# Kernel tuning notes

Measured on AMD Instinct MI355X. Metric: run time of the kernel, lower is better.

The kernel has to match this reference:

```python
import jax, jax.numpy as jnp
import numpy as np
from math import factorial, sqrt

E_EDGES = 65536
N_NODES = 4096
F_HID = 64
MUL = 64
EPSILON = 0.25
P_ENV = 6.0

# ---- real Clebsch-Gordan (e3nn-style w3j, unit Frobenius norm) ----

def _su2_cg(j1, j2, j3, m1, m2, m3):
    if m3 != m1 + m2:
        return 0.0
    f = factorial
    pref = sqrt((2 * j3 + 1) * f(j3 + j1 - j2) * f(j3 - j1 + j2) * f(j1 + j2 - j3) / f(j1 + j2 + j3 + 1))
    pref *= sqrt(f(j3 + m3) * f(j3 - m3) * f(j1 - m1) * f(j1 + m1) * f(j2 - m2) * f(j2 + m2))
    s = 0.0
    for k in range(0, j1 + j2 - j3 + 1):
        d = [k, j1 + j2 - j3 - k, j1 - m1 - k, j2 + m2 - k, j3 - j2 + m1 + k, j3 - j1 - m2 + k]
        if min(d) < 0:
            continue
        den = 1.0
        for t in d:
            den *= f(t)
        s += (-1.0) ** k / den
    return pref * s

def _qmat(l):  # real -> complex change of basis, [complex m, real m]
    q = np.zeros((2 * l + 1, 2 * l + 1), dtype=np.complex128)
    for m in range(-l, 0):
        q[l + m, l + abs(m)] = 1.0 / sqrt(2)
        q[l + m, l - abs(m)] = -1j / sqrt(2)
    q[l, l] = 1.0
    for m in range(1, l + 1):
        q[l + m, l + abs(m)] = (-1) ** m / sqrt(2)
        q[l + m, l - abs(m)] = 1j * (-1) ** m / sqrt(2)
    return (-1j) ** l * q

def _w3j(l1, l2, l3):
    C = np.zeros((2 * l1 + 1, 2 * l2 + 1, 2 * l3 + 1), dtype=np.complex128)
    for i, m1 in enumerate(range(-l1, l1 + 1)):
        for j, m2 in enumerate(range(-l2, l2 + 1)):
            for k, m3 in enumerate(range(-l3, l3 + 1)):
                C[i, j, k] = _su2_cg(l1, l2, l3, m1, m2, m3)
    Cr = np.einsum('ai,bj,ck,abc->ijk', _qmat(l1), _qmat(l2), np.conj(_qmat(l3)), C)
    Cr = np.real(Cr)
    return (Cr / np.linalg.norm(Cr)).astype(np.float32)

_PATH_KEYS = [(0,0,0),(1,1,0),(2,2,0),(0,1,1),(1,0,1),(1,2,1),(2,1,1),(3,2,1),(0,2,2),(1,1,2),(2,0,2),(2,2,2),(3,1,2),(2,1,3)]
_W3J_NP = {k: _w3j(*k) for k in _PATH_KEYS}

def _sh_consts():  # normalization so ||Y_l||^2 = 2l+1 (component norm)
    u = np.array([0.3, -0.4, sqrt(0.75)])
    y1 = sqrt(3.0) * u
    y2r = np.einsum('i,j,ijk->k', y1, y1, _W3J_NP[(1, 1, 2)])
    c2 = sqrt(5.0) / np.linalg.norm(y2r)
    y3r = np.einsum('i,j,ijk->k', c2 * y2r, y1, _W3J_NP[(2, 1, 3)])
    c3 = sqrt(7.0) / np.linalg.norm(y3r)
    return float(c2), float(c3)

_C2, _C3 = _sh_consts()
_W3J = {k: jnp.asarray(v) for k, v in _W3J_NP.items()}


def _sph(u):  # component-normalized real SH l=0..3 via CG recursion, u unit [E,3]
    y0 = jnp.ones_like(u[:, :1])
    y1 = jnp.sqrt(jnp.float32(3.0)) * u
    y2 = _C2 * jnp.einsum('ei,ej,ijk->ek', y1, y1, _W3J[(1, 1, 2)])
    y3 = _C3 * jnp.einsum('ei,ej,ijk->ek', y2, y1, _W3J[(2, 1, 3)])
    return jnp.concatenate([y0, y1, y2, y3], axis=1)  # [E, 16]


def _tp(a, b, key):  # per-mul CG product path, component normalization
    l3 = key[2]
    return jnp.sqrt(jnp.float32(2 * l3 + 1)) * jnp.einsum('eui,euj,ijk->euk', a, b, _W3J[key])


def _forward(vectors, x, V, Ww, W1, W2, W3, Wl1, Wl2, senders):
    E = vectors.shape[0]
    lengths = jnp.linalg.norm(vectors, axis=1)  # [E]
    u = vectors / (lengths[:, None] + 1e-12)
    Y = _sph(u)  # [E, 16]
    # two-body MLP (single linear, no act), e3nn 1/sqrt(fan_in) scaling
    w = (x @ Ww) / jnp.sqrt(jnp.float32(x.shape[1]))  # [E, MUL]
    # weighted SH, scatter_sum over senders, map back to edges
    M = w[:, :, None] * Y[:, None, :]  # [E, MUL, 16]
    wY = jax.ops.segment_sum(M, senders, num_segments=N_NODES)[senders] * EPSILON
    wY0, wY1, wY2, wY3 = wY[..., 0:1], wY[..., 1:4], wY[..., 4:9], wY[..., 9:16]
    V0 = V[:, :MUL].reshape(E, MUL, 1)
    V1 = V[:, MUL:4 * MUL].reshape(E, MUL, 3)
    V2 = V[:, 4 * MUL:9 * MUL].reshape(E, MUL, 5)
    # CG tensor product wY(0e+1o+2e+3o) x V(0e+1o+2e), filtered to 0e+1o+2e
    S = jnp.concatenate([_tp(wY0, V0, (0, 0, 0)), _tp(wY1, V1, (1, 1, 0)), _tp(wY2, V2, (2, 2, 0))], axis=1)[..., 0]  # [E, 3*MUL]
    P = jnp.concatenate([_tp(wY0, V1, (0, 1, 1)), _tp(wY1, V0, (1, 0, 1)), _tp(wY1, V2, (1, 2, 1)), _tp(wY2, V1, (2, 1, 1)), _tp(wY3, V2, (3, 2, 1))], axis=1)  # [E, 5*MUL, 3]
    D = jnp.concatenate([_tp(wY0, V2, (0, 2, 2)), _tp(wY1, V1, (1, 1, 2)), _tp(wY2, V0, (2, 0, 2)), _tp(wY2, V2, (2, 2, 2)), _tp(wY3, V1, (3, 1, 2))], axis=1)  # [E, 5*MUL, 5]
    # scalars join the invariant track; latent MLP (silu x2, last linear)
    h = jnp.concatenate([x, S], axis=1)  # [E, F_HID + 3*MUL]
    h = jax.nn.silu(h @ W1 / jnp.sqrt(jnp.float32(h.shape[1])))
    h = jax.nn.silu(h @ W2 / jnp.sqrt(jnp.float32(F_HID)))
    h = h @ W3 / jnp.sqrt(jnp.float32(F_HID))
    # polynomial smoothing envelope (cutoff = 1)
    p = P_ENV
    d = lengths
    env = 1.0 - (p + 1.0) * (p + 2.0) / 2.0 * d ** 6 + p * (p + 2.0) * d ** 7 - p * (p + 1.0) / 2.0 * d ** 8
    env = jnp.where(d < 1.0, env, 0.0)
    x_out = env[:, None] * h  # [E, F_HID]
    # equivariant Linear to 64x1o + 64x2e (0e dropped: no path)
    nin = jnp.sqrt(jnp.float32(P.shape[1]))
    V1o = jnp.einsum('evi,vu->eui', P, Wl1) / nin  # [E, MUL, 3]
    V2e = jnp.einsum('evi,vu->eui', D, Wl2) / nin  # [E, MUL, 5]
    return jnp.concatenate([x_out, V1o.reshape(E, 3 * MUL), V2e.reshape(E, 5 * MUL)], axis=1)  # [E, 576]


def setup_inputs() -> dict:
    key = jax.random.key(0)
    ks = jax.random.split(key, 11)
    v = jax.random.normal(ks[0], (E_EDGES, 3), dtype=jnp.float32)
    r = 0.2 + 0.75 * jax.random.uniform(ks[1], (E_EDGES, 1), dtype=jnp.float32)
    vectors = v / (jnp.linalg.norm(v, axis=1, keepdims=True) + 1e-9) * r  # lengths in (0.2, 0.95)
    x = jax.random.normal(ks[2], (E_EDGES, F_HID), dtype=jnp.float32)
    V = jax.random.normal(ks[3], (E_EDGES, 9 * MUL), dtype=jnp.float32)
    senders = jax.random.randint(ks[4], (E_EDGES,), 0, N_NODES)
    Ww = jax.random.normal(ks[5], (F_HID, MUL), dtype=jnp.float32)
    W1 = jax.random.normal(ks[6], (F_HID + 3 * MUL, F_HID), dtype=jnp.float32)
    W2 = jax.random.normal(ks[7], (F_HID, F_HID), dtype=jnp.float32)
    W3 = jax.random.normal(ks[8], (F_HID, F_HID), dtype=jnp.float32)
    Wl1 = jax.random.normal(ks[9], (5 * MUL, MUL), dtype=jnp.float32)
    Wl2 = jax.random.normal(ks[10], (5 * MUL, MUL), dtype=jnp.float32)
    return {"vectors": vectors, "x": x, "V": V, "senders": senders, "Ww": Ww, "W1": W1, "W2": W2, "W3": W3, "Wl1": Wl1, "Wl2": Wl2}


def reference(vectors, x, V, senders, Ww, W1, W2, W3, Wl1, Wl2):
    return _forward(vectors, x, V, Ww, W1, W2, W3, Wl1, Wl2, senders)
```

## Files before the change

kernel.cpp:

```cpp
#include <hip/hip_runtime.h>

#define E_EDGES 65536
#define N_NODES 4096

#define WS_W     1024
#define WS_Y     (WS_W + E_EDGES*64)
#define WS_CNT   (WS_Y + E_EDGES*16)
#define WS_OFF   (WS_CNT + N_NODES)
#define WS_CUR   (WS_OFF + N_NODES)
#define WS_SORT  (WS_CUR + N_NODES)
#define WS_A     (WS_SORT + E_EDGES)

typedef __bf16 bf16x8 __attribute__((ext_vector_type(8)));
typedef float  f32x4  __attribute__((ext_vector_type(4)));

#define PK_WL   0
#define PK_W1   10240
#define PK_W2   14336
#define PK_W3   15360

__constant__ int gK_L1[14] = {0,1,2,0,1,1,2,3,0,1,2,2,3,2};
__constant__ int gK_L2[14] = {0,1,2,1,0,2,1,2,2,1,0,2,1,1};
__constant__ int gK_L3[14] = {0,0,0,1,1,1,1,1,2,2,2,2,2,3};
__constant__ int gK_OFF[14]= {0,1,10,35,44,53,98,143,248,273,318,343,468,573};
__constant__ double gFact[8] = {1.,1.,2.,6.,24.,120.,720.,5040.};

#define O_W000 0
#define O_W110 1
#define O_W220 10
#define O_W011 35
#define O_W101 44
#define O_W121 53
#define O_W211 98
#define O_W321 143
#define O_W022 248
#define O_W112 273
#define O_W202 318
#define O_W222 343
#define O_W312 468
#define O_W213 573

__device__ double su2_cg(int j1,int j2,int j3,int m1,int m2,int m3){
  if (m3 != m1+m2) return 0.0;
  double pref = sqrt((double)(2*j3+1)*gFact[j3+j1-j2]*gFact[j3-j1+j2]*gFact[j1+j2-j3]/gFact[j1+j2+j3+1]);
  pref *= sqrt(gFact[j3+m3]*gFact[j3-m3]*gFact[j1-m1]*gFact[j1+m1]*gFact[j2-m2]*gFact[j2+m2]);
  double s=0.0;
  for(int k=0;k<=j1+j2-j3;k++){
    int d1=j1+j2-j3-k, d2=j1-m1-k, d3=j2+m2-k, d4=j3-j2+m1+k, d5=j3-j1-m2+k;
    if(d1<0||d2<0||d3<0||d4<0||d5<0) continue;
    double den=gFact[k]*gFact[d1]*gFact[d2]*gFact[d3]*gFact[d4]*gFact[d5];
    s += (k&1)? (-1.0/den) : (1.0/den);
  }
  return pref*s;
}

__device__ void fill_qmat(int l, double2* q){
  for(int i=0;i<49;i++){ q[i].x=0.0; q[i].y=0.0; }
  const double is2 = 0.7071067811865475244;
  for(int m=-l;m<0;m++){
    q[(l+m)*7+(l-m)].x = is2;
    q[(l+m)*7+(l+m)].y = -is2;
  }
  q[l*7+l].x = 1.0;
  for(int m=1;m<=l;m++){
    double sg = (m&1)? -1.0 : 1.0;
    q[(l+m)*7+(l+m)].x = sg*is2;
    q[(l+m)*7+(l-m)].y = sg*is2;
  }
  double pr, pi;
  switch(l&3){ case 0: pr=1;pi=0;break; case 1: pr=0;pi=-1;break; case 2: pr=-1;pi=0;break; default: pr=0;pi=1;break; }
  for(int i=0;i<49;i++){
    double a=q[i].x, b=q[i].y;
    q[i].x = a*pr - b*pi;
    q[i].y = a*pi + b*pr;
  }
}

__global__ __launch_bounds__(128) void k_w3j(float* __restrict__ ws){
  __shared__ double2 q1[49], q2[49], q3[49];
  __shared__ double C[125], Cr[125];
  __shared__ double red[128];
  int bid = blockIdx.x, t = threadIdx.x;
  int l1=gK_L1[bid], l2=gK_L2[bid], l3=gK_L3[bid];
  int n1=2*l1+1, n2=2*l2+1, n3=2*l3+1, ntot=n1*n2*n3;
  if(t==0){
    fill_qmat(l1,q1); fill_qmat(l2,q2); fill_qmat(l3,q3);
    for(int i=0;i<49;i++) q3[i].y = -q3[i].y;
  }
  __syncthreads();
  for(int idx=t; idx<ntot; idx+=128){
    int a = idx/(n2*n3), r=idx%(n2*n3), b=r/n3, c=r%n3;
    C[idx] = su2_cg(l1,l2,l3, a-l1, b-l2, c-l3);
  }
  __syncthreads();
  for(int idx=t; idx<ntot; idx+=128){
    int i = idx/(n2*n3), r=idx%(n2*n3), j=r/n3, k=r%n3;
    double ar=0.0;
    for(int a=0;a<n1;a++) for(int b=0;b<n2;b++){
      double2 qa=q1[a*7+i], qb=q2[b*7+j];
      double pr = qa.x*qb.x - qa.y*qb.y;
      double pi = qa.x*qb.y + qa.y*qb.x;
      for(int c=0;c<n3;c++){
        double2 qc=q3[c*7+k];
        double tr = pr*qc.x - pi*qc.y;
        ar += tr*C[(a*n2+b)*n3+c];
      }
    }
    Cr[idx]=ar;
  }
  __syncthreads();
  double ss=0.0;
  for(int idx=t; idx<ntot; idx+=128) ss += Cr[idx]*Cr[idx];
  red[t]=ss; __syncthreads();
  for(int st=64; st>0; st>>=1){ if(t<st) red[t]+=red[t+st]; __syncthreads(); }
  double inv = 1.0/sqrt(red[0]);
  for(int idx=t; idx<ntot; idx+=128) ws[gK_OFF[bid]+idx] = (float)(Cr[idx]*inv);
}

__global__ void k_c2c3(float* __restrict__ ws){
  const float* w112 = ws + O_W112;
  const float* w213 = ws + O_W213;
  double u0=0.3, u1=-0.4, u2=sqrt(0.75);
  double s3=sqrt(3.0);
  double y1[3]={s3*u0, s3*u1, s3*u2};
  double y2r[5]={0,0,0,0,0};
  for(int i=0;i<3;i++) for(int j=0;j<3;j++) for(int k=0;k<5;k++)
    y2r[k] += y1[i]*y1[j]*(double)w112[(i*3+j)*5+k];
  double nn=0; for(int k=0;k<5;k++) nn += y2r[k]*y2r[k];
  double c2 = sqrt(5.0)/sqrt(nn);
  double y2[5]; for(int k=0;k<5;k++) y2[k]=c2*y2r[k];
  double y3r[7]={0,0,0,0,0,0,0};
  for(int i=0;i<5;i++) for(int j=0;j<3;j++) for(int n=0;n<7;n++)
    y3r[n] += y2[i]*y1[j]*(double)w213[(i*3+j)*7+n];
  nn=0; for(int n=0;n<7;n++) nn += y3r[n]*y3r[n];
  double c3 = sqrt(7.0)/sqrt(nn);
  ws[678]=(float)c2; ws[679]=(float)c3;
}

__global__ void k_zero(int* __restrict__ cnt){
  int i = blockIdx.x*256 + threadIdx.x;
  if(i < N_NODES) cnt[i]=0;
}
__global__ void k_count(const int* __restrict__ senders, int* __restrict__ cnt){
  int e = blockIdx.x*256 + threadIdx.x;
  if(e < E_EDGES) atomicAdd(&cnt[senders[e]], 1);
}
__global__ __launch_bounds__(1024) void k_scan(const int* __restrict__ cnt, int* __restrict__ off, int* __restrict__ cur){
  __shared__ int part[1024];
  int t = threadIdx.x;
  int c0=cnt[4*t], c1=cnt[4*t+1], c2=cnt[4*t+2], c3=cnt[4*t+3];
  int l0=0, l1=c0, l2=c0+c1, l3=c0+c1+c2;
  int sum=l3+c3;
  part[t]=sum; __syncthreads();
  for(int st=1; st<1024; st<<=1){
    int v = part[t];
    int add = (t>=st)? part[t-st] : 0;
    __syncthreads();
    part[t] = v + add;
    __syncthreads();
  }
  int pref = (t>0)? part[t-1] : 0;
  off[4*t]=pref+l0; off[4*t+1]=pref+l1; off[4*t+2]=pref+l2; off[4*t+3]=pref+l3;
  cur[4*t]=pref+l0; cur[4*t+1]=pref+l1; cur[4*t+2]=pref+l2; cur[4*t+3]=pref+l3;
}
__global__ void k_scatter(const int* __restrict__ senders, int* __restrict__ cur, int* __restrict__ sorted){
  int e = blockIdx.x*256 + threadIdx.x;
  if(e < E_EDGES){
    int pos = atomicAdd(&cur[senders[e]], 1);
    sorted[pos] = e;
  }
}

__global__ __launch_bounds__(256) void k_wpack(
    const float* __restrict__ Wl1, const float* __restrict__ Wl2,
    const float* __restrict__ W1, const float* __restrict__ W2,
    const float* __restrict__ W3, float* __restrict__ wpk){
  int idx = blockIdx.x*256 + threadIdx.x;
  int lane = idx & 63;
  const float* W; int part, ks, nt;
  if(idx < PK_W1){
    nt = (idx>>6)&3; int rest = idx>>8; ks = rest%10; int mp = rest/10;
    part = mp&1; W = (mp>>1)? Wl2 : Wl1;
  } else if(idx < PK_W2){
    int rel = idx - PK_W1; part = rel>>11; int r2 = rel & 2047;
    ks = r2>>8; nt = (r2>>6)&3; W = W1;
  } else if(idx < PK_W3){
    int rel = idx - PK_W2; part = rel>>9; int r2 = rel & 511;
    ks = r2>>8; nt = (r2>>6)&3; W = W2;
  } else {
    int rel = idx - PK_W3; part = rel>>9; int r2 = rel & 511;
    ks = r2>>8; nt = (r2>>6)&3; W = W3;
  }
  int c = nt*16 + (lane & 15);
  int g = lane >> 4;
  bf16x8 outv;
  #pragma unroll
  for(int j=0;j<8;j++){
    int k = ks*32 + g*8 + j;
    float v = W[k*64 + c];
    __bf16 hb = (__bf16)v;
    outv[j] = part ? (__bf16)(v - (float)hb) : hb;
  }
  ((bf16x8*)wpk)[idx] = outv;
}

__global__ __launch_bounds__(256) void k_edge_pre(
    const float* __restrict__ vectors, const float* __restrict__ x,
    const float* __restrict__ Ww, float* __restrict__ ws){
  int wv = threadIdx.x >> 6, lane = threadIdx.x & 63;
  int e = blockIdx.x*4 + wv;
  const float* w112 = ws + O_W112;
  const float* w213 = ws + O_W213;
  float C2v = ws[678], C3v = ws[679];
  float v0=vectors[e*3], v1=vectors[e*3+1], v2=vectors[e*3+2];
  float len = sqrtf(v0*v0+v1*v1+v2*v2);
  float inv = 1.0f/(len + 1e-12f);
  float s3 = 1.7320508075688772f;
  float y1v[3] = { s3*v0*inv, s3*v1*inv, s3*v2*inv };
  float y2[5];
  #pragma unroll
  for(int k=0;k<5;k++){
    float a=0.f;
    #pragma unroll
    for(int i=0;i<3;i++)
      #pragma unroll
      for(int j=0;j<3;j++) a += y1v[i]*y1v[j]*w112[(i*3+j)*5+k];
    y2[k]=C2v*a;
  }
  float y3[7];
  #pragma unroll
  for(int n=0;n<7;n++){
    float a=0.f;
    #pragma unroll
    for(int i=0;i<5;i++)
      #pragma unroll
      for(int j=0;j<3;j++) a += y2[i]*y1v[j]*w213[(i*3+j)*7+n];
    y3[n]=C3v*a;
  }
  float acc=0.f;
  const float4* xp4 = (const float4*)(x + e*64);
  #pragma unroll
  for(int k4=0;k4<16;k4++){
    float4 xv = xp4[k4];
    acc += xv.x*Ww[(k4*4+0)*64+lane];
    acc += xv.y*Ww[(k4*4+1)*64+lane];
    acc += xv.z*Ww[(k4*4+2)*64+lane];
    acc += xv.w*Ww[(k4*4+3)*64+lane];
  }
  ws[WS_W + e*64 + lane] = acc*0.125f;
  if(lane==0){
    float* Yp = ws + WS_Y + e*16;
    Yp[0]=1.0f;
    Yp[1]=y1v[0]; Yp[2]=y1v[1]; Yp[3]=y1v[2];
    Yp[4]=y2[0]; Yp[5]=y2[1]; Yp[6]=y2[2]; Yp[7]=y2[3]; Yp[8]=y2[4];
    Yp[9]=y3[0]; Yp[10]=y3[1]; Yp[11]=y3[2]; Yp[12]=y3[3]; Yp[13]=y3[4]; Yp[15]=y3[6]; Yp[14]=y3[5];
  }
}

__global__ __launch_bounds__(64) void k_node_acc(
    const float* __restrict__ ws_w, const float* __restrict__ ws_y,
    const int* __restrict__ sorted, const int* __restrict__ off, const int* __restrict__ cnt,
    float* __restrict__ A){
  int n = blockIdx.x, m = threadIdx.x;
  float acc[16];
  #pragma unroll
  for(int k=0;k<16;k++) acc[k]=0.f;
  int o = off[n], c = cnt[n];
  for(int j=0;j<c;j++){
    int e = sorted[o+j];
    float wm = ws_w[e*64+m];
    const float4* Yp4 = (const float4*)(ws_y + e*16);
    float4 y0=Yp4[0], y1=Yp4[1], y2=Yp4[2], y3=Yp4[3];
    acc[0] += wm*y0.x; acc[1] += wm*y0.y; acc[2] += wm*y0.z; acc[3] += wm*y0.w;
    acc[4] += wm*y1.x; acc[5] += wm*y1.y; acc[6] += wm*y1.z; acc[7] += wm*y1.w;
    acc[8] += wm*y2.x; acc[9] += wm*y2.y; acc[10]+= wm*y2.z; acc[11]+= wm*y2.w;
    acc[12]+= wm*y3.x; acc[13]+= wm*y3.y; acc[14]+= wm*y3.z; acc[15]+= wm*y3.w;
  }
  float4* outp = (float4*)(A + n*1024 + m*16);
  outp[0] = make_float4(acc[0]*0.25f, acc[1]*0.25f, acc[2]*0.25f, acc[3]*0.25f);
  outp[1] = make_float4(acc[4]*0.25f, acc[5]*0.25f, acc[6]*0.25f, acc[7]*0.25f);
  outp[2] = make_float4(acc[8]*0.25f, acc[9]*0.25f, acc[10]*0.25f, acc[11]*0.25f);
  outp[3] = make_float4(acc[12]*0.25f, acc[13]*0.25f, acc[14]*0.25f, acc[15]*0.25f);
}

__device__ inline void split1(float v, __bf16& h, __bf16& l){
  h = (__bf16)v;
  l = (__bf16)(v - (float)h);
}

__global__ __launch_bounds__(256, 3) void k_main(
    const float* __restrict__ vectors, const float* __restrict__ x, const float* __restrict__ V,
    const int* __restrict__ senders,
    const float* __restrict__ ws, const int* __restrict__ sorted,
    float* __restrict__ out){
  __shared__ __align__(16) __bf16 lds_pdh[32*328];
  __shared__ __align__(16) __bf16 lds_pdl[32*328];
  __shared__ __align__(16) __bf16 lds_hh[4*264];
  __shared__ __align__(16) __bf16 lds_hl[4*264];
  __shared__ __align__(16) __bf16 lds_h1h[4*72];
  __shared__ __align__(16) __bf16 lds_h1l[4*72];
  __shared__ __align__(16) __bf16 lds_h2h[4*72];
  __shared__ __align__(16) __bf16 lds_h2l[4*72];
  __shared__ float lds_env[4];
  __shared__ int   lds_eid[4];

  int t = threadIdx.x;
  int wv = t>>6, lane = t&63;
  int eid = sorted[blockIdx.x*4 + wv];
  if(lane==0) lds_eid[wv]=eid;
  __syncthreads();

  const float* lw = ws;
  {
    float v0=vectors[eid*3], v1=vectors[eid*3+1], v2=vectors[eid*3+2];
    float d = sqrtf(v0*v0+v1*v1+v2*v2);
    float d2=d*d, d4=d2*d2, d6=d4*d2, d7=d6*d, d8=d7*d;
    float env = 1.0f - 28.0f*d6 + 48.0f*d7 - 21.0f*d8;
    env = (d < 1.0f) ? env : 0.0f;
    if(lane==0) lds_env[wv]=env;
  }
  int snd = senders[eid];
  const float4* Ap4 = (const float4*)(ws + WS_A + snd*1024 + lane*16);
  float4 a0=Ap4[0], a1=Ap4[1], a2=Ap4[2], a3=Ap4[3];
  float wY[16] = {a0.x,a0.y,a0.z,a0.w, a1.x,a1.y,a1.z,a1.w,
                  a2.x,a2.y,a2.z,a2.w, a3.x,a3.y,a3.z,a3.w};
  const float* Vp = V + eid*576;
  float V0 = Vp[lane];
  float V1f[3], V2f[5];
  #pragma unroll
  for(int i=0;i<3;i++) V1f[i]=Vp[64+lane*3+i];
  #pragma unroll
  for(int j=0;j<5;j++) V2f[j]=Vp[256+lane*5+j];
  {
    __bf16 hh, hl;
    split1(x[eid*64+lane], hh, hl);
    lds_hh[wv*264 + lane] = hh; lds_hl[wv*264 + lane] = hl;
  }
  float s0 = wY[0]*V0*lw[O_W000];
  float s1 = 0.f;
  #pragma unroll
  for(int i=0;i<3;i++)
    #pragma unroll
    for(int j=0;j<3;j++) s1 += wY[1+i]*V1f[j]*lw[O_W110 + i*3+j];
  float s2 = 0.f;
  #pragma unroll
  for(int i=0;i<5;i++)
    #pragma unroll
    for(int j=0;j<5;j++) s2 += wY[4+i]*V2f[j]*lw[O_W220 + i*5+j];
  {
    __bf16 hh, hl;
    split1(s0, hh, hl); lds_hh[wv*264+ 64+lane]=hh; lds_hl[wv*264+ 64+lane]=hl;
    split1(s1, hh, hl); lds_hh[wv*264+128+lane]=hh; lds_hl[wv*264+128+lane]=hl;
    split1(s2, hh, hl); lds_hh[wv*264+192+lane]=hh; lds_hl[wv*264+192+lane]=hl;
  }
  float P0[3]={0,0,0}, P1[3]={0,0,0}, P2[3]={0,0,0}, P3[3]={0,0,0}, P4[3]={0,0,0};
  float D0[5]={0,0,0,0,0}, D1[5]={0,0,0,0,0}, D2[5]={0,0,0,0,0}, D3[5]={0,0,0,0,0}, D4[5]={0,0,0,0,0};
  #pragma unroll
  for(int b=0;b<3;b++){ float pb=wY[0]*V1f[b];
    #pragma unroll
    for(int i=0;i<3;i++) P0[i]+= pb*lw[O_W011 + b*3+i]; }
  #pragma unroll
  for(int a=0;a<3;a++){ float pa=wY[1+a]*V0;
    #pragma unroll
    for(int i=0;i<3;i++) P1[i]+= pa*lw[O_W101 + a*3+i]; }
  #pragma unroll
  for(int a=0;a<3;a++)
    #pragma unroll
    for(int b=0;b<5;b++){ float p=wY[1+a]*V2f[b];
      #pragma unroll
      for(int i=0;i<3;i++) P2[i]+= p*lw[O_W121 + (a*5+b)*3+i]; }
  #pragma unroll
  for(int a=0;a<5;a++)
    #pragma unroll
    for(int b=0;b<3;b++){ float p=wY[4+a]*V1f[b];
      #pragma unroll
      for(int i=0;i<3;i++) P3[i]+= p*lw[O_W211 + (a*3+b)*3+i]; }
  #pragma unroll
  for(int a=0;a<7;a++)
    #pragma unroll
    for(int b=0;b<5;b++){ float p=wY[9+a]*V2f[b];
      #pragma unroll
      for(int i=0;i<3;i++) P4[i]+= p*lw[O_W321 + (a*5+b)*3+i]; }
  #pragma unroll
  for(int b=0;b<5;b++){ float pb=wY[0]*V2f[b];
    #pragma unroll
    for(int j=0;j<5;j++) D0[j]+= pb*lw[O_W022 + b*5+j]; }
  #pragma unroll
  for(int a=0;a<3;a++)
    #pragma unroll
    for(int b=0;b<3;b++){ float p=wY[1+a]*V1f[b];
      #pragma unroll
      for(int j=0;j<5;j++) D1[j]+= p*lw[O_W112 + (a*3+b)*5+j]; }
  #pragma unroll
  for(int a=0;a<5;a++){ float pa=wY[4+a]*V0;
    #pragma unroll
    for(int j=0;j<5;j++) D2[j]+= pa*lw[O_W202 + a*5+j]; }
  #pragma unroll
  for(int a=0;a<5;a++)
    #pragma unroll
    for(int b=0;b<5;b++){ float p=wY[4+a]*V2f[b];
      #pragma unroll
      for(int j=0;j<5;j++) D3[j]+= p*lw[O_W222 + (a*5+b)*5+j]; }
  #pragma unroll
  for(int a=0;a<7;a++)
    #pragma unroll
    for(int b=0;b<3;b++){ float p=wY[9+a]*V1f[b];
      #pragma unroll
      for(int j=0;j<5;j++) D4[j]+= p*lw[O_W312 + (a*3+b)*5+j]; }
  {
    const float SQ3 = 1.7320508075688772f, SQ5 = 2.2360679774997896f;
    #pragma unroll
    for(int i=0;i<3;i++){
      int row = wv*3+i;
      float vals[5] = {SQ3*P0[i], SQ3*P1[i], SQ3*P2[i], SQ3*P3[i], SQ3*P4[i]};
      #pragma unroll
      for(int p=0;p<5;p++){
        __bf16 h,l; split1(vals[p],h,l);
        lds_pdh[row*328 + p*64 + lane] = h;
        lds_pdl[row*328 + p*64 + lane] = l;
      }
    }
    #pragma unroll
    for(int j=0;j<5;j++){
      int row = 12 + wv*5 + j;
      float vals[5] = {SQ5*D0[j], SQ5*D1[j], SQ5*D2[j], SQ5*D3[j], SQ5*D4[j]};
      #pragma unroll
      for(int p=0;p<5;p++){
        __bf16 h,l; split1(vals[p],h,l);
        lds_pdh[row*328 + p*64 + lane] = h;
        lds_pdl[row*328 + p*64 + lane] = l;
      }
    }
  }
  __syncthreads();

  int g = lane >> 4, r = lane & 15;
  const bf16x8* WB = (const bf16x8*)(ws + WS_W);

  {
    int he = r & 3;
    f32x4 acc = {0.f,0.f,0.f,0.f};
    #pragma unroll
    for(int ks=0; ks<8; ks++){
      bf16x8 ah = *(const bf16x8*)(lds_hh + he*264 + ks*32 + g*8);
      bf16x8 al = *(const bf16x8*)(lds_hl + he*264 + ks*32 + g*8);
      bf16x8 bh = WB[PK_W1        + (ks*4+wv)*64 + lane];
      bf16x8 bl = WB[PK_W1 + 2048 + (ks*4+wv)*64 + lane];
      acc = __builtin_amdgcn_mfma_f32_16x16x32_bf16(ah, bh, acc, 0,0,0);
      acc = __builtin_amdgcn_mfma_f32_16x16x32_bf16(ah, bl, acc, 0,0,0);
      acc = __builtin_amdgcn_mfma_f32_16x16x32_bf16(al, bh, acc, 0,0,0);
    }
    if(g==0){
      #pragma unroll
      for(int e_=0;e_<4;e_++){
        float a = acc[e_]*(1.0f/16.0f);
        float h1 = a/(1.0f+__expf(-a));
        __bf16 hh,hl; split1(h1,hh,hl);
        lds_h1h[e_*72 + wv*16 + r] = hh;
        lds_h1l[e_*72 + wv*16 + r] = hl;
      }
    }
    __syncthreads();
    acc = (f32x4){0.f,0.f,0.f,0.f};
    #pragma unroll
    for(int ks=0; ks<2; ks++){
      bf16x8 ah = *(const bf16x8*)(lds_h1h + he*72 + ks*32 + g*8);
      bf16x8 al = *(const bf16x8*)(lds_h1l + he*72 + ks*32 + g*8);
      bf16x8 bh = WB[PK_W2       + (ks*4+wv)*64 + lane];
      bf16x8 bl = WB[PK_W2 + 512 + (ks*4+wv)*64 + lane];
      acc = __builtin_amdgcn_mfma_f32_16x16x32_bf16(ah, bh, acc, 0,0,0);
      acc = __builtin_amdgcn_mfma_f32_16x16x32_bf16(ah, bl, acc, 0,0,0);
      acc = __builtin_amdgcn_mfma_f32_16x16x32_bf16(al, bh, acc, 0,0,0);
    }
    if(g==0){
      #pragma unroll
      for(int e_=0;e_<4;e_++){
        float a = acc[e_]*0.125f;
        float h2 = a/(1.0f+__expf(-a));
        __bf16 hh,hl; split1(h2,hh,hl);
        lds_h2h[e_*72 + wv*16 + r] = hh;
        lds_h2l[e_*72 + wv*16 + r] = hl;
      }
    }
    __syncthreads();
    acc = (f32x4){0.f,0.f,0.f,0.f};
    #pragma unroll
    for(int ks=0; ks<2; ks++){
      bf16x8 ah = *(const bf16x8*)(lds_h2h + he*72 + ks*32 + g*8);
      bf16x8 al = *(const bf16x8*)(lds_h2l + he*72 + ks*32 + g*8);
      bf16x8 bh = WB[PK_W3       + (ks*4+wv)*64 + lane];
      bf16x8 bl = WB[PK_W3 + 512 + (ks*4+wv)*64 + lane];
      acc = __builtin_amdgcn_mfma_f32_16x16x32_bf16(ah, bh, acc, 0,0,0);
      acc = __builtin_amdgcn_mfma_f32_16x16x32_bf16(ah, bl, acc, 0,0,0);
      acc = __builtin_amdgcn_mfma_f32_16x16x32_bf16(al, bh, acc, 0,0,0);
    }
    if(g==0){
      #pragma unroll
      for(int e_=0;e_<4;e_++)
        out[lds_eid[e_]*576 + wv*16 + r] = lds_env[e_]*acc[e_]*0.125f;
    }
  }

  {
    f32x4 accP  = {0.f,0.f,0.f,0.f};
    f32x4 accD0 = {0.f,0.f,0.f,0.f};
    f32x4 accD1 = {0.f,0.f,0.f,0.f};
    int rP  = (r < 12) ? r : 11;
    int rD0 = 12 + r;
    int rD1 = 12 + ((r < 4) ? (16 + r) : 19);
    const __bf16* pPh  = lds_pdh + rP *328 + g*8;
    const __bf16* pPl  = lds_pdl + rP *328 + g*8;
    const __bf16* pD0h = lds_pdh + rD0*328 + g*8;
    const __bf16* pD0l = lds_pdl + rD0*328 + g*8;
    const __bf16* pD1h = lds_pdh + rD1*328 + g*8;
    const __bf16* pD1l = lds_pdl + rD1*328 + g*8;
    #pragma unroll 2
    for(int ks=0; ks<10; ks++){
      int bbase = (ks*4 + wv)*64 + lane;
      bf16x8 b1h = WB[bbase];
      bf16x8 b1l = WB[bbase + 2560];
      bf16x8 b2h = WB[bbase + 5120];
      bf16x8 b2l = WB[bbase + 7680];
      bf16x8 aPh  = *(const bf16x8*)(pPh  + ks*32);
      bf16x8 aPl  = *(const bf16x8*)(pPl  + ks*32);
      bf16x8 aD0h = *(const bf16x8*)(pD0h + ks*32);
      bf16x8 aD0l = *(const bf16x8*)(pD0l + ks*32);
      bf16x8 aD1h = *(const bf16x8*)(pD1h + ks*32);
      bf16x8 aD1l = *(const bf16x8*)(pD1l + ks*32);
      accP  = __builtin_amdgcn_mfma_f32_16x16x32_bf16(aPh,  b1h, accP,  0,0,0);
      accP  = __builtin_amdgcn_mfma_f32_16x16x32_bf16(aPh,  b1l, accP,  0,0,0);
      accP  = __builtin_amdgcn_mfma_f32_16x16x32_bf16(aPl,  b1h, accP,  0,0,0);
      accD0 = __builtin_amdgcn_mfma_f32_16x16x32_bf16(aD0h, b2h, accD0, 0,0,0);
      accD0 = __builtin_amdgcn_mfma_f32_16x16x32_bf16(aD0h, b2l, accD0, 0,0,0);
      accD0 = __builtin_amdgcn_mfma_f32_16x16x32_bf16(aD0l, b2h, accD0, 0,0,0);
      accD1 = __builtin_amdgcn_mfma_f32_16x16x32_bf16(aD1h, b2h, accD1, 0,0,0);
      accD1 = __builtin_amdgcn_mfma_f32_16x16x32_bf16(aD1h, b2l, accD1, 0,0,0);
      accD1 = __builtin_amdgcn_mfma_f32_16x16x32_bf16(aD1l, b2h, accD1, 0,0,0);
    }
    const float sc = 0.05590169943749474f;
    int u = wv*16 + r;
    if(g < 3){
      #pragma unroll
      for(int reg=0; reg<4; reg++){
        int R = g*4 + reg;
        int e_ = R/3, i_ = R - e_*3;
        out[lds_eid[e_]*576 + 64 + u*3 + i_] = accP[reg]*sc;
      }
    }
    #pragma unroll
    for(int reg=0; reg<4; reg++){
      int Dr = g*4 + reg;
      int e_ = Dr/5, j_ = Dr - e_*5;
      out[lds_eid[e_]*576 + 256 + u*5 + j_] = accD0[reg]*sc;
    }
    if(g == 0){
      #pragma unroll
      for(int reg=0; reg<4; reg++){
        int Dr = 16 + reg;
        int e_ = Dr/5, j_ = Dr - e_*5;
        out[lds_eid[e_]*576 + 256 + u*5 + j_] = accD1[reg]*sc;
      }
    }
  }
}

extern "C" void kernel_launch(void* const* d_in, const int* in_sizes, int n_in,
                              void* d_out, int out_size, void* d_ws, size_t ws_size,
                              hipStream_t stream) {
  const float* vectors=(const float*)d_in[0];
  const float* x      =(const float*)d_in[1];
  const float* V      =(const float*)d_in[2];
  const int*   senders=(const int*)  d_in[3];
  const float* Ww     =(const float*)d_in[4];
  const float* W1     =(const float*)d_in[5];
  const float* W2     =(const float*)d_in[6];
  const float* W3     =(const float*)d_in[7];
  const float* Wl1    =(const float*)d_in[8];
  const float* Wl2    =(const float*)d_in[9];
  float* ws  = (float*)d_ws;
  float* out = (float*)d_out;
  int* cnt    = (int*)(ws + WS_CNT);
  int* off    = (int*)(ws + WS_OFF);
  int* cur    = (int*)(ws + WS_CUR);
  int* sorted = (int*)(ws + WS_SORT);

  k_w3j   <<<14, 128, 0, stream>>>(ws);
  k_c2c3  <<<1, 1, 0, stream>>>(ws);
  k_zero  <<<16, 256, 0, stream>>>(cnt);
  k_count <<<E_EDGES/256, 256, 0, stream>>>(senders, cnt);
  k_scan  <<<1, 1024, 0, stream>>>(cnt, off, cur);
  k_scatter<<<E_EDGES/256, 256, 0, stream>>>(senders, cur, sorted);
  k_edge_pre<<<E_EDGES/4, 256, 0, stream>>>(vectors, x, Ww, ws);
  k_node_acc<<<N_NODES, 64, 0, stream>>>(ws + WS_W, ws + WS_Y, sorted, off, cnt, ws + WS_A);
  k_wpack <<<64, 256, 0, stream>>>(Wl1, Wl2, W1, W2, W3, ws + WS_W);
  k_main  <<<E_EDGES/4, 256, 0, stream>>>(vectors, x, V, senders,
                                          ws, sorted, out);
}
```

Measured before the change: 645.8 us.

## Compute edge Ww projection with split-bf16 MFMA and prefetch node edge indices

Replaces the scalar FP32 x·Ww dot product in the edge precompute kernel with 16x16x32 bf16 MFMA calls. Both operands are split into high and low bf16 parts so the result stays close to FP32 accuracy. A new small kernel pre-packs Ww into that split layout in the cur scratch region, which is no longer needed after scatter, and folds the c2/c3 constant computation into its spare block to drop one launch. The node accumulation loop now loads the next sorted edge index one iteration ahead to hide index-load latency. The split-bf16 scheme costs three MFMAs per k-step, and reusing the cur buffer depends on scatter having finished first.

```diff
diff --git a/kernel.cpp b/kernel.cpp
--- a/kernel.cpp
+++ b/kernel.cpp
@@ -117,7 +117,7 @@
   for(int idx=t; idx<ntot; idx+=128) ws[gK_OFF[bid]+idx] = (float)(Cr[idx]*inv);
 }
 
-__global__ void k_c2c3(float* __restrict__ ws){
+__device__ void do_c2c3(float* ws){
   const float* w112 = ws + O_W112;
   const float* w213 = ws + O_W213;
   double u0=0.3, u1=-0.4, u2=sqrt(0.75);
@@ -169,6 +169,26 @@
     int pos = atomicAdd(&cur[senders[e]], 1);
     sorted[pos] = e;
   }
+}
+
+__global__ __launch_bounds__(256) void k_wwpack(const float* __restrict__ Ww, float* __restrict__ ws){
+  if(blockIdx.x == 4){
+    if(threadIdx.x == 0) do_c2c3(ws);
+    return;
+  }
+  int idx = blockIdx.x*256 + threadIdx.x;
+  int lane = idx & 63, nt = (idx>>6)&3, ks = (idx>>8)&1, part = idx>>9;
+  int c = nt*16 + (lane & 15);
+  int g = lane >> 4;
+  bf16x8 outv;
+  #pragma unroll
+  for(int j=0;j<8;j++){
+    int k = ks*32 + g*8 + j;
+    float v = Ww[k*64 + c];
+    __bf16 hb = (__bf16)v;
+    outv[j] = part ? (__bf16)(v - (float)hb) : hb;
+  }
+  ((bf16x8*)(ws + WS_CUR))[idx] = outv;
 }
 
 __global__ __launch_bounds__(256) void k_wpack(
@@ -204,10 +224,16 @@
   ((bf16x8*)wpk)[idx] = outv;
 }
 
+__device__ inline void split1(float v, __bf16& h, __bf16& l){
+  h = (__bf16)v;
+  l = (__bf16)(v - (float)h);
+}
+
 __global__ __launch_bounds__(256) void k_edge_pre(
     const float* __restrict__ vectors, const float* __restrict__ x,
-    const float* __restrict__ Ww, float* __restrict__ ws){
-  int wv = threadIdx.x >> 6, lane = threadIdx.x & 63;
+    float* __restrict__ ws){
+  int t = threadIdx.x;
+  int wv = t >> 6, lane = t & 63;
   int e = blockIdx.x*4 + wv;
   const float* w112 = ws + O_W112;
   const float* w213 = ws + O_W213;
@@ -237,17 +263,32 @@
       for(int j=0;j<3;j++) a += y2[i]*y1v[j]*w213[(i*3+j)*7+n];
     y3[n]=C3v*a;
   }
-  float acc=0.f;
-  const float4* xp4 = (const float4*)(x + e*64);
-  #pragma unroll
-  for(int k4=0;k4<16;k4++){
-    float4 xv = xp4[k4];
-    acc += xv.x*Ww[(k4*4+0)*64+lane];
-    acc += xv.y*Ww[(k4*4+1)*64+lane];
-    acc += xv.z*Ww[(k4*4+2)*64+lane];
-    acc += xv.w*Ww[(k4*4+3)*64+lane];
-  }
-  ws[WS_W + e*64 + lane] = acc*0.125f;
+  {
+    int g = lane >> 4, r = lane & 15, he = r & 3;
+    const float* xrow = x + (blockIdx.x*4 + he)*64;
+    const bf16x8* WWP = (const bf16x8*)(ws + WS_CUR);
+    f32x4 acc = {0.f,0.f,0.f,0.f};
+    #pragma unroll
+    for(int ks=0; ks<2; ks++){
+      const float* xp = xrow + ks*32 + g*8;
+      bf16x8 ah, al;
+      #pragma unroll
+      for(int j=0;j<8;j++){
+        __bf16 h,l; split1(xp[j],h,l);
+        ah[j]=h; al[j]=l;
+      }
+      bf16x8 bh = WWP[      ks*256 + wv*64 + lane];
+      bf16x8 bl = WWP[512 + ks*256 + wv*64 + lane];
+      acc = __builtin_amdgcn_mfma_f32_16x16x32_bf16(ah, bh, acc, 0,0,0);
+      acc = __builtin_amdgcn_mfma_f32_16x16x32_bf16(ah, bl, acc, 0,0,0);
+      acc = __builtin_amdgcn_mfma_f32_16x16x32_bf16(al, bh, acc, 0,0,0);
+    }
+    if(g==0){
+      #pragma unroll
+      for(int reg=0; reg<4; reg++)
+        ws[WS_W + (blockIdx.x*4+reg)*64 + wv*16 + r] = acc[reg]*0.125f;
+    }
+  }
   if(lane==0){
     float* Yp = ws + WS_Y + e*16;
     Yp[0]=1.0f;
@@ -266,26 +307,25 @@
   #pragma unroll
   for(int k=0;k<16;k++) acc[k]=0.f;
   int o = off[n], c = cnt[n];
-  for(int j=0;j<c;j++){
-    int e = sorted[o+j];
-    float wm = ws_w[e*64+m];
-    const float4* Yp4 = (const float4*)(ws_y + e*16);
-    float4 y0=Yp4[0], y1=Yp4[1], y2=Yp4[2], y3=Yp4[3];
-    acc[0] += wm*y0.x; acc[1] += wm*y0.y; acc[2] += wm*y0.z; acc[3] += wm*y0.w;
-    acc[4] += wm*y1.x; acc[5] += wm*y1.y; acc[6] += wm*y1.z; acc[7] += wm*y1.w;
-    acc[8] += wm*y2.x; acc[9] += wm*y2.y; acc[10]+= wm*y2.z; acc[11]+= wm*y2.w;
-    acc[12]+= wm*y3.x; acc[13]+= wm*y3.y; acc[14]+= wm*y3.z; acc[15]+= wm*y3.w;
+  if(c > 0){
+    int e = sorted[o];
+    for(int j=0;j<c;j++){
+      int e_nx = (j+1<c) ? sorted[o+j+1] : 0;
+      float wm = ws_w[e*64+m];
+      const float4* Yp4 = (const float4*)(ws_y + e*16);
+      float4 y0=Yp4[0], y1=Yp4[1], y2=Yp4[2], y3=Yp4[3];
+      acc[0] += wm*y0.x; acc[1] += wm*y0.y; acc[2] += wm*y0.z; acc[3] += wm*y0.w;
+      acc[4] += wm*y1.x; acc[5] += wm*y1.y; acc[6] += wm*y1.z; acc[7] += wm*y1.w;
+      acc[8] += wm*y2.x; acc[9] += wm*y2.y; acc[10]+= wm*y2.z; acc[11]+= wm*y2.w;
+      acc[12]+= wm*y3.x; acc[13]+= wm*y3.y; acc[14]+= wm*y3.z; acc[15]+= wm*y3.w;
+      e = e_nx;
+    }
   }
   float4* outp = (float4*)(A + n*1024 + m*16);
   outp[0] = make_float4(acc[0]*0.25f, acc[1]*0.25f, acc[2]*0.25f, acc[3]*0.25f);
   outp[1] = make_float4(acc[4]*0.25f, acc[5]*0.25f, acc[6]*0.25f, acc[7]*0.25f);
   outp[2] = make_float4(acc[8]*0.25f, acc[9]*0.25f, acc[10]*0.25f, acc[11]*0.25f);
   outp[3] = make_float4(acc[12]*0.25f, acc[13]*0.25f, acc[14]*0.25f, acc[15]*0.25f);
-}
-
-__device__ inline void split1(float v, __bf16& h, __bf16& l){
-  h = (__bf16)v;
-  l = (__bf16)(v - (float)h);
 }
 
 __global__ __launch_bounds__(256, 3) void k_main(
@@ -585,12 +625,12 @@
   int* sorted = (int*)(ws + WS_SORT);
 
   k_w3j   <<<14, 128, 0, stream>>>(ws);
-  k_c2c3  <<<1, 1, 0, stream>>>(ws);
   k_zero  <<<16, 256, 0, stream>>>(cnt);
   k_count <<<E_EDGES/256, 256, 0, stream>>>(senders, cnt);
   k_scan  <<<1, 1024, 0, stream>>>(cnt, off, cur);
   k_scatter<<<E_EDGES/256, 256, 0, stream>>>(senders, cur, sorted);
-  k_edge_pre<<<E_EDGES/4, 256, 0, stream>>>(vectors, x, Ww, ws);
+  k_wwpack<<<5, 256, 0, stream>>>(Ww, ws);
+  k_edge_pre<<<E_EDGES/4, 256, 0, stream>>>(vectors, x, ws);
   k_node_acc<<<N_NODES, 64, 0, stream>>>(ws + WS_W, ws + WS_Y, sorted, off, cnt, ws + WS_A);
   k_wpack <<<64, 256, 0, stream>>>(Wl1, Wl2, W1, W2, W3, ws + WS_W);
   k_main  <<<E_EDGES/4, 256, 0, stream>>>(vectors, x, V, senders,
```

After: 621.8 us. 1.04x faster.
